# Performance work log

Hardware: AMD Instinct MI355X
Metric: run time of the kernel (lower is better)

## Reference

```python
import jax, jax.numpy as jnp
import numpy as np

D = 16      # core_size
R = 8       # rank
SIZE = D ** 3  # 4096, nr_cores = 3


def setup_inputs() -> dict:
    key = jax.random.key(0)
    k = jax.random.split(key, 5)
    core_std = np.sqrt(2.0 / D).astype(np.float32)  # kaiming_normal over (-1, d, d)
    x = jax.random.normal(k[0], (8, 1024, SIZE), dtype=jnp.float32)
    core0 = core_std * jax.random.normal(k[1], (D, D, D, D, R, 1), dtype=jnp.float32)
    core1 = core_std * jax.random.normal(k[2], (D, D, D, D, R, R), dtype=jnp.float32)
    core2 = core_std * jax.random.normal(k[3], (D, D, D, D, 1, R), dtype=jnp.float32)
    bias = np.sqrt(1.0 / SIZE).astype(np.float32) * jax.random.uniform(
        k[4], (SIZE,), dtype=jnp.float32, minval=-1.0, maxval=1.0)
    return {"x": x, "core0": core0, "core1": core1, "core2": core2, "bias": bias}


def to_matrix(core0, core1, core2):
    # Faithful translation of BTT.to_matrix for nr_cores=3.
    # G starts as core0: (d,d,d,d,r,1)
    # step idx=0 (core1): j=d, i=d^2
    c1 = core1.reshape(D, D * D, D, R, R)          # jixcb
    g = core0.reshape(D, D * D, D, R, 1)           # jiyba
    G = jnp.einsum('jixcb,jiyba->jiyxca', c1, g)   # (d, d^2, d, d, r, 1)
    # step idx=1 (core2): j=d^2, i=d
    c2 = core2.reshape(D * D, D, D, 1, R)          # jixcb
    g = G.reshape(D * D, D, D * D, R, 1)           # jiyba
    G = jnp.einsum('jixcb,jiyba->jiyxca', c2, g)   # (d^2, d, d^2, d, 1, 1)
    return G.reshape(SIZE, SIZE)


def reference(x, core0, core1, core2, bias):
    G = to_matrix(core0, core1, core2)
    out = x.reshape(-1, SIZE) @ G + bias
    return out.reshape(x.shape)
```

## Files before the change

kernel.cpp:

```cpp
#include <hip/hip_runtime.h>
#include <stdint.h>

typedef unsigned short u16;
typedef short bf16x8 __attribute__((ext_vector_type(8)));
typedef float f32x4 __attribute__((ext_vector_type(4)));
typedef u16 u16x4 __attribute__((ext_vector_type(4)));

__device__ __forceinline__ u16 f2bf(float f) {
    union { float f; unsigned int i; } v; v.f = f;
    unsigned int x = v.i;
    return (u16)((x + 0x7FFFu + ((x >> 16) & 1u)) >> 16);
}

__device__ __forceinline__ void async_load16(const u16* g, u16* lds) {
    __builtin_amdgcn_global_load_lds(
        (const __attribute__((address_space(1))) unsigned int*)g,
        (__attribute__((address_space(3))) unsigned int*)lds,
        16, 0, 0);
}

__global__ void transpose_cores(const float* __restrict__ c0, const float* __restrict__ c1,
                                const float* __restrict__ c2, float* __restrict__ c0t,
                                float* __restrict__ c1t, float* __restrict__ c2t) {
    __shared__ float t[64][65];
    int b = blockIdx.x;
    const float* in; float* outp; int Q, qt, rt;
    if (b < 1024)      { in = c1; outp = c1t; Q = 1024; qt = b & 15;          rt = b >> 4; }
    else if (b < 1152) { b -= 1024; in = c0; outp = c0t; Q = 128; qt = b & 1; rt = b >> 1; }
    else               { b -= 1152; in = c2; outp = c2t; Q = 128; qt = b & 1; rt = b >> 1; }
    const int r0 = rt * 64, q0 = qt * 64;
    const int tx = threadIdx.x & 63, ty = threadIdx.x >> 6;
    #pragma unroll
    for (int k = 0; k < 16; ++k)
        t[k * 4 + ty][tx] = in[(size_t)(r0 + k * 4 + ty) * Q + q0 + tx];
    __syncthreads();
    #pragma unroll
    for (int k = 0; k < 16; ++k)
        outp[(size_t)(q0 + k * 4 + ty) * 4096 + r0 + tx] = t[tx][k * 4 + ty];
}

__global__ __launch_bounds__(256, 1)
void build_gt_reuse(const float* __restrict__ c0t, const float* __restrict__ c1t,
                    const float* __restrict__ c2t, u16* __restrict__ Gt) {
    const int x1 = blockIdx.x;
    const int r  = blockIdx.y * 256 + threadIdx.x;

    float c1v[64];
    #pragma unroll
    for (int q = 0; q < 64; ++q)
        c1v[q] = c1t[(size_t)(x1 * 64 + q) * 4096 + r];

    #pragma unroll
    for (int yh = 0; yh < 2; ++yh) {
        float t[8][8];
        #pragma unroll
        for (int yy = 0; yy < 8; ++yy) {
            const int y1 = yh * 8 + yy;
            float a0[8];
            #pragma unroll
            for (int b = 0; b < 8; ++b)
                a0[b] = c0t[(size_t)(y1 * 8 + b) * 4096 + r];
            #pragma unroll
            for (int c = 0; c < 8; ++c) {
                float s = 0.f;
                #pragma unroll
                for (int b = 0; b < 8; ++b) s += c1v[c * 8 + b] * a0[b];
                t[yy][c] = s;
            }
        }
        #pragma unroll
        for (int x2 = 0; x2 < 16; ++x2) {
            float c2v[8];
            #pragma unroll
            for (int c = 0; c < 8; ++c)
                c2v[c] = c2t[(size_t)(x2 * 8 + c) * 4096 + r];
            #pragma unroll
            for (int yy = 0; yy < 8; ++yy) {
                const int y1 = yh * 8 + yy;
                float s = 0.f;
                #pragma unroll
                for (int c = 0; c < 8; ++c) s += c2v[c] * t[yy][c];
                Gt[(size_t)((y1 * 16 + x1) * 16 + x2) * 4096 + r] = f2bf(s);
            }
        }
    }
}

__global__ void conv_x(const f32x4* __restrict__ x, u16* __restrict__ xb, int n4) {
    for (int i = blockIdx.x * 256 + threadIdx.x; i < n4; i += gridDim.x * 256) {
        f32x4 v = x[i];
        u16x4 o;
        #pragma unroll
        for (int j = 0; j < 4; ++j) o[j] = f2bf(v[j]);
        *(u16x4*)(xb + 4 * (size_t)i) = o;
    }
}

__global__ __launch_bounds__(512, 2)
void gemm_8ph(const u16* __restrict__ Xb, const u16* __restrict__ Gt,
              const float* __restrict__ bias, float* __restrict__ out) {
    constexpr int K = 4096, N = 4096, NT = 64;
    extern __shared__ u16 lds[];

    const int tid  = threadIdx.x;
    const int lane = tid & 63;
    const int w    = tid >> 6;
    const int wmi  = w >> 2;
    const int wni  = w & 3;
    const int lr   = lane & 15;
    const int lq   = lane >> 4;
    const int xr   = lr & 7;

    int id = blockIdx.y * 16 + blockIdx.x;
    id = (id & 7) * 64 + (id >> 3);
    const int m0 = (id & 31) * 256;
    const int n0 = (id >> 5) * 256;

    const int r0 = tid >> 3;
    const int s0 = (tid & 7) ^ (r0 & 7);
    const int r1 = 64 + r0;
    const int s1 = ((512 + tid) & 7) ^ (r1 & 7);
    const size_t aoff0 = (size_t)(m0 + r0) * K + s0 * 8;
    const size_t aoff1 = (size_t)(m0 + r1) * K + s1 * 8;
    const size_t boff0 = (size_t)(n0 + r0) * K + s0 * 8;
    const size_t boff1 = (size_t)(n0 + r1) * K + s1 * 8;
    const int ldsw0 = (tid & ~63) * 8;
    const int ldsw1 = 4096 + (tid & ~63) * 8;

    const int aoffL = (wmi * 16 + lr) * 64;
    const int boffL = 16384 + (wni * 16 + lr) * 64;
    const int slot0 = (lq ^ xr) * 8;
    const int slot1 = ((4 + lq) ^ xr) * 8;

    f32x4 acc[8][4] = {};
    bf16x8 a[4][2];
    bf16x8 bfr[2][2][2];

    auto stageA = [&](int bb, int h, int t) {
        const u16* s = Xb + (size_t)h * (128 * K) + (size_t)t * 64;
        u16* d = lds + bb * 32768 + h * 8192;
        async_load16(s + aoff0, d + ldsw0);
        async_load16(s + aoff1, d + ldsw1);
    };
    auto stageB = [&](int bb, int h, int t) {
        const u16* s = Gt + (size_t)h * (128 * K) + (size_t)t * 64;
        u16* d = lds + bb * 32768 + 16384 + h * 8192;
        async_load16(s + boff0, d + ldsw0);
        async_load16(s + boff1, d + ldsw1);
    };
    auto loadA = [&](int bb, int h) {
        const u16* p = lds + bb * 32768 + h * 8192 + aoffL;
        #pragma unroll
        for (int li = 0; li < 4; ++li) {
            a[li][0] = *(const bf16x8*)(p + li * 2048 + slot0);
            a[li][1] = *(const bf16x8*)(p + li * 2048 + slot1);
        }
    };
    auto loadB = [&](int bb, int h) {
        const u16* p = lds + bb * 32768 + h * 8192 + boffL;
        #pragma unroll
        for (int lj = 0; lj < 2; ++lj) {
            bfr[h][lj][0] = *(const bf16x8*)(p + lj * 4096 + slot0);
            bfr[h][lj][1] = *(const bf16x8*)(p + lj * 4096 + slot1);
        }
    };
    auto mfmaQ = [&](int mh, int nh) {
        #pragma unroll
        for (int li = 0; li < 4; ++li)
            #pragma unroll
            for (int lj = 0; lj < 2; ++lj) {
                f32x4 c = acc[mh * 4 + li][nh * 2 + lj];
                c = __builtin_amdgcn_mfma_f32_16x16x32_bf16(a[li][0], bfr[nh][lj][0], c, 0, 0, 0);
                c = __builtin_amdgcn_mfma_f32_16x16x32_bf16(a[li][1], bfr[nh][lj][1], c, 0, 0, 0);
                acc[mh * 4 + li][nh * 2 + lj] = c;
            }
    };
    auto mfmaQ_refillA = [&](int mh, int nh, const u16* pA) {
        #pragma unroll
        for (int li = 0; li < 4; ++li) {
            #pragma unroll
            for (int lj = 0; lj < 2; ++lj) {
                f32x4 c = acc[mh * 4 + li][nh * 2 + lj];
                c = __builtin_amdgcn_mfma_f32_16x16x32_bf16(a[li][0], bfr[nh][lj][0], c, 0, 0, 0);
                c = __builtin_amdgcn_mfma_f32_16x16x32_bf16(a[li][1], bfr[nh][lj][1], c, 0, 0, 0);
                acc[mh * 4 + li][nh * 2 + lj] = c;
            }
            a[li][0] = *(const bf16x8*)(pA + li * 2048 + slot0);
            a[li][1] = *(const bf16x8*)(pA + li * 2048 + slot1);
        }
    };

    stageA(0, 0, 0); stageB(0, 0, 0); stageA(0, 1, 0); stageB(0, 1, 0);
    stageA(1, 0, 1); stageB(1, 0, 1); stageA(1, 1, 1); stageB(1, 1, 1);
    asm volatile("s_waitcnt vmcnt(8)" ::: "memory");
    __builtin_amdgcn_s_barrier();
    loadB(0, 1); loadA(0, 0); loadB(0, 0);

    for (int T = 0; T < NT; ++T) {
        const int bc = T & 1, bn = bc ^ 1;
        const int t2 = (T + 2) & (NT - 1);

        asm volatile("s_waitcnt lgkmcnt(0)" ::: "memory");
        __builtin_amdgcn_s_barrier();
        __builtin_amdgcn_sched_barrier(0);
        __builtin_amdgcn_s_setprio(1);
        mfmaQ(0, 0);
        __builtin_amdgcn_s_setprio(0);

        stageA(bc, 0, t2); stageB(bc, 0, t2);
        __builtin_amdgcn_s_setprio(1);
        mfmaQ_refillA(0, 1, lds + bc * 32768 + 8192 + aoffL);
        __builtin_amdgcn_s_setprio(0);

        asm volatile("s_waitcnt lgkmcnt(0)" ::: "memory");
        __builtin_amdgcn_s_barrier();
        __builtin_amdgcn_sched_barrier(0);
        __builtin_amdgcn_s_setprio(1);
        mfmaQ(1, 1);
        __builtin_amdgcn_s_setprio(0);

        stageA(bc, 1, t2); stageB(bc, 1, t2);
        asm volatile("s_waitcnt vmcnt(8)" ::: "memory");
        __builtin_amdgcn_s_barrier();
        __builtin_amdgcn_sched_barrier(0);
        loadB(bn, 1);
        __builtin_amdgcn_s_setprio(1);
        mfmaQ_refillA(1, 0, lds + bn * 32768 + aoffL);
        __builtin_amdgcn_s_setprio(0);
        loadB(bn, 0);
    }
    asm volatile("s_waitcnt vmcnt(0) lgkmcnt(0)" ::: "memory");

    #pragma unroll
    for (int j = 0; j < 4; ++j) {
        const int n = n0 + (j * 4 + wni) * 16 + lr;
        const float bv = bias[n];
        #pragma unroll
        for (int i = 0; i < 8; ++i) {
            const int mb = m0 + (2 * i + wmi) * 16 + lq * 4;
            #pragma unroll
            for (int r = 0; r < 4; ++r)
                out[(size_t)(mb + r) * N + n] = acc[i][j][r] + bv;
        }
    }
}

__global__ void build_gt(const float* __restrict__ c0, const float* __restrict__ c1,
                         const float* __restrict__ c2, u16* __restrict__ Gt) {
    const int y1  = blockIdx.x >> 4;
    const int x1  = blockIdx.x & 15;
    const int r   = blockIdx.y * 256 + threadIdx.x;

    float a0[8];
    {
        f32x4 v0 = *(const f32x4*)(c0 + ((size_t)r * 16 + y1) * 8);
        f32x4 v1 = *(const f32x4*)(c0 + ((size_t)r * 16 + y1) * 8 + 4);
        #pragma unroll
        for (int b = 0; b < 4; ++b) { a0[b] = v0[b]; a0[4 + b] = v1[b]; }
    }
    float t[8];
    const float* c1row = c1 + ((size_t)r * 16 + x1) * 64;
    #pragma unroll
    for (int c = 0; c < 8; ++c) {
        f32x4 v0 = *(const f32x4*)(c1row + c * 8);
        f32x4 v1 = *(const f32x4*)(c1row + c * 8 + 4);
        float s = 0.f;
        #pragma unroll
        for (int b = 0; b < 4; ++b) s += v0[b] * a0[b] + v1[b] * a0[4 + b];
        t[c] = s;
    }
    const float* c2row = c2 + (size_t)r * 128;
    #pragma unroll
    for (int x2 = 0; x2 < 16; ++x2) {
        f32x4 v0 = *(const f32x4*)(c2row + x2 * 8);
        f32x4 v1 = *(const f32x4*)(c2row + x2 * 8 + 4);
        float s = 0.f;
        #pragma unroll
        for (int c = 0; c < 4; ++c) s += v0[c] * t[c] + v1[c] * t[4 + c];
        Gt[((size_t)(blockIdx.x * 16 + x2)) * 4096 + r] = f2bf(s);
    }
}

#define TM 128
#define TN 128
#define BK 32

__global__ void gemm_bt_f32(const float* __restrict__ Xf, const u16* __restrict__ Gt,
                            const float* __restrict__ bias, float* __restrict__ out) {
    constexpr int K = 4096, N = 4096;
    __shared__ __attribute__((aligned(16))) u16 As[TM * BK];
    __shared__ __attribute__((aligned(16))) u16 Bs[TN * BK];

    const int tid  = threadIdx.x;
    const int lane = tid & 63;
    const int w    = tid >> 6;
    const int m0   = blockIdx.y * TM;
    const int n0   = blockIdx.x * TN;
    const int wm   = (w >> 1) * 64;
    const int wn   = (w & 1) * 64;
    const int lr   = lane & 15;
    const int lk   = (lane >> 4) * 8;

    f32x4 acc[4][4] = {};

    const int srow   = tid >> 2;
    const int schunk = (tid & 3) * 8;
    const u16* grow0 = Gt + (size_t)(n0 + srow) * K + schunk;
    const u16* grow1 = Gt + (size_t)(n0 + 64 + srow) * K + schunk;
    u16* ldsB0 = &Bs[(tid & ~63) * 8];
    u16* ldsB1 = &Bs[(256 + (tid & ~63)) * 8];

    const float* xsrc = Xf + (size_t)(m0 + (tid >> 1)) * K + (tid & 1) * 16;
    u16* adst = &As[(tid >> 1) * BK + (tid & 1) * 16];

    for (int k0 = 0; k0 < K; k0 += BK) {
        __syncthreads();
        {
            f32x4 v0 = ((const f32x4*)(xsrc + k0))[0];
            f32x4 v1 = ((const f32x4*)(xsrc + k0))[1];
            f32x4 v2 = ((const f32x4*)(xsrc + k0))[2];
            f32x4 v3 = ((const f32x4*)(xsrc + k0))[3];
            bf16x8 w0, w1;
            #pragma unroll
            for (int j = 0; j < 4; ++j) {
                w0[j]     = (short)f2bf(v0[j]);
                w0[4 + j] = (short)f2bf(v1[j]);
                w1[j]     = (short)f2bf(v2[j]);
                w1[4 + j] = (short)f2bf(v3[j]);
            }
            *(bf16x8*)adst = w0;
            *(bf16x8*)(adst + 8) = w1;
        }
        async_load16(grow0 + k0, ldsB0);
        async_load16(grow1 + k0, ldsB1);
        __syncthreads();

        bf16x8 af[4], bg[4];
        #pragma unroll
        for (int i = 0; i < 4; ++i) {
            af[i] = *(const bf16x8*)(&As[(wm + i * 16 + lr) * BK + lk]);
            bg[i] = *(const bf16x8*)(&Bs[(wn + i * 16 + lr) * BK + lk]);
        }
        #pragma unroll
        for (int mt = 0; mt < 4; ++mt)
            #pragma unroll
            for (int nt = 0; nt < 4; ++nt)
                acc[mt][nt] = __builtin_amdgcn_mfma_f32_16x16x32_bf16(
                    af[mt], bg[nt], acc[mt][nt], 0, 0, 0);
    }

    #pragma unroll
    for (int nt = 0; nt < 4; ++nt) {
        const int n = n0 + wn + nt * 16 + lr;
        const float bv = bias[n];
        #pragma unroll
        for (int mt = 0; mt < 4; ++mt) {
            const int mbase = m0 + wm + mt * 16 + (lane >> 4) * 4;
            #pragma unroll
            for (int r = 0; r < 4; ++r) {
                out[(size_t)(mbase + r) * N + n] = acc[mt][nt][r] + bv;
            }
        }
    }
}

extern "C" void kernel_launch(void* const* d_in, const int* in_sizes, int n_in,
                              void* d_out, int out_size, void* d_ws, size_t ws_size,
                              hipStream_t stream) {
    const float* x    = (const float*)d_in[0];
    const float* c0   = (const float*)d_in[1];
    const float* c1   = (const float*)d_in[2];
    const float* c2   = (const float*)d_in[3];
    const float* bias = (const float*)d_in[4];
    float* out = (float*)d_out;

    const size_t GT_BYTES   = (size_t)4096 * 4096 * sizeof(u16);
    const size_t XB_BYTES   = (size_t)8192 * 4096 * sizeof(u16);
    const size_t CORE_BYTES = (size_t)20 * 1024 * 1024;
    u16* Gt = (u16*)d_ws;

    if (ws_size >= GT_BYTES + XB_BYTES) {
        u16* Xb = (u16*)((char*)d_ws + GT_BYTES);
        static int attr_done = 0;
        if (!attr_done) {
            hipFuncSetAttribute(reinterpret_cast<const void*>(gemm_8ph),
                                hipFuncAttributeMaxDynamicSharedMemorySize, 131072);
            attr_done = 1;
        }

        float* c1t; float* c0t; float* c2t;
        if (ws_size >= GT_BYTES + XB_BYTES + CORE_BYTES) {
            char* cores = (char*)d_ws + GT_BYTES + XB_BYTES;
            c1t = (float*)cores;
            c0t = (float*)(cores + (size_t)16 * 1024 * 1024);
            c2t = (float*)(cores + (size_t)18 * 1024 * 1024);
        } else {
            char* scratch = (char*)d_ws + GT_BYTES;
            c1t = (float*)scratch;
            c0t = (float*)(scratch + (size_t)16 * 1024 * 1024);
            c2t = (float*)(scratch + (size_t)18 * 1024 * 1024);
        }
        transpose_cores<<<1280, 256, 0, stream>>>(c0, c1, c2, c0t, c1t, c2t);
        build_gt_reuse<<<dim3(16, 16), 256, 0, stream>>>(c0t, c1t, c2t, Gt);
        conv_x<<<8192, 256, 0, stream>>>((const f32x4*)x, Xb, 8192 * 4096 / 4);
        gemm_8ph<<<dim3(16, 32), 512, 131072, stream>>>(Xb, Gt, bias, out);
    } else {
        build_gt<<<dim3(256, 16), 256, 0, stream>>>(c0, c1, c2, Gt);
        gemm_bt_f32<<<dim3(32, 64), 256, 0, stream>>>(x, Gt, bias, out);
    }
}
```

Measured before the change: 498.1 us.

## Restructure LDS fragment loads to overlap with MFMA and move barriers after compute

Splits the A-fragment LDS reads into two halves. The second half and the B high fragment are now issued at the start of each quadrant instead of being waited on before a barrier. The waitcnt/barrier pairs move after the MFMA quadrants so LDS reads overlap with matrix math rather than stalling before it. This adds register pressure and depends on the compiler keeping MFMA and LDS reads interleaved without the sched_barrier fences. It could also introduce hazards if a buffer is overwritten before the moved barriers are reached.

```diff
diff --git a/kernel.cpp b/kernel.cpp
--- a/kernel.cpp
+++ b/kernel.cpp
@@ -148,13 +148,17 @@
         async_load16(s + boff0, d + ldsw0);
         async_load16(s + boff1, d + ldsw1);
     };
-    auto loadA = [&](int bb, int h) {
-        const u16* p = lds + bb * 32768 + h * 8192 + aoffL;
-        #pragma unroll
-        for (int li = 0; li < 4; ++li) {
-            a[li][0] = *(const bf16x8*)(p + li * 2048 + slot0);
-            a[li][1] = *(const bf16x8*)(p + li * 2048 + slot1);
-        }
+    auto loadA01 = [&](const u16* pA) {
+        a[0][0] = *(const bf16x8*)(pA + slot0);
+        a[0][1] = *(const bf16x8*)(pA + slot1);
+        a[1][0] = *(const bf16x8*)(pA + 2048 + slot0);
+        a[1][1] = *(const bf16x8*)(pA + 2048 + slot1);
+    };
+    auto loadA23 = [&](const u16* pA) {
+        a[2][0] = *(const bf16x8*)(pA + 2 * 2048 + slot0);
+        a[2][1] = *(const bf16x8*)(pA + 2 * 2048 + slot1);
+        a[3][0] = *(const bf16x8*)(pA + 3 * 2048 + slot0);
+        a[3][1] = *(const bf16x8*)(pA + 3 * 2048 + slot1);
     };
     auto loadB = [&](int bb, int h) {
         const u16* p = lds + bb * 32768 + h * 8192 + boffL;
@@ -175,7 +179,7 @@
                 acc[mh * 4 + li][nh * 2 + lj] = c;
             }
     };
-    auto mfmaQ_refillA = [&](int mh, int nh, const u16* pA) {
+    auto mfmaQ_r01 = [&](int mh, int nh, const u16* pA) {
         #pragma unroll
         for (int li = 0; li < 4; ++li) {
             #pragma unroll
@@ -185,8 +189,10 @@
                 c = __builtin_amdgcn_mfma_f32_16x16x32_bf16(a[li][1], bfr[nh][lj][1], c, 0, 0, 0);
                 acc[mh * 4 + li][nh * 2 + lj] = c;
             }
-            a[li][0] = *(const bf16x8*)(pA + li * 2048 + slot0);
-            a[li][1] = *(const bf16x8*)(pA + li * 2048 + slot1);
+            if (li < 2) {
+                a[li][0] = *(const bf16x8*)(pA + li * 2048 + slot0);
+                a[li][1] = *(const bf16x8*)(pA + li * 2048 + slot1);
+            }
         }
     };
 
@@ -194,38 +200,40 @@
     stageA(1, 0, 1); stageB(1, 0, 1); stageA(1, 1, 1); stageB(1, 1, 1);
     asm volatile("s_waitcnt vmcnt(8)" ::: "memory");
     __builtin_amdgcn_s_barrier();
-    loadB(0, 1); loadA(0, 0); loadB(0, 0);
+    loadA01(lds + aoffL);
+    loadB(0, 0);
 
     for (int T = 0; T < NT; ++T) {
         const int bc = T & 1, bn = bc ^ 1;
         const int t2 = (T + 2) & (NT - 1);
-
-        asm volatile("s_waitcnt lgkmcnt(0)" ::: "memory");
-        __builtin_amdgcn_s_barrier();
-        __builtin_amdgcn_sched_barrier(0);
+        const u16* pc = lds + bc * 32768;
+
+        loadB(bc, 1);
+        loadA23(pc + aoffL);
         __builtin_amdgcn_s_setprio(1);
         mfmaQ(0, 0);
         __builtin_amdgcn_s_setprio(0);
+        asm volatile("s_waitcnt lgkmcnt(0)" ::: "memory");
+        __builtin_amdgcn_s_barrier();
 
         stageA(bc, 0, t2); stageB(bc, 0, t2);
         __builtin_amdgcn_s_setprio(1);
-        mfmaQ_refillA(0, 1, lds + bc * 32768 + 8192 + aoffL);
+        mfmaQ_r01(0, 1, pc + 8192 + aoffL);
         __builtin_amdgcn_s_setprio(0);
 
-        asm volatile("s_waitcnt lgkmcnt(0)" ::: "memory");
-        __builtin_amdgcn_s_barrier();
-        __builtin_amdgcn_sched_barrier(0);
+        loadA23(pc + 8192 + aoffL);
         __builtin_amdgcn_s_setprio(1);
         mfmaQ(1, 1);
         __builtin_amdgcn_s_setprio(0);
+        asm volatile("s_waitcnt lgkmcnt(0)" ::: "memory");
+        __builtin_amdgcn_s_barrier();
 
         stageA(bc, 1, t2); stageB(bc, 1, t2);
         asm volatile("s_waitcnt vmcnt(8)" ::: "memory");
         __builtin_amdgcn_s_barrier();
         __builtin_amdgcn_sched_barrier(0);
-        loadB(bn, 1);
         __builtin_amdgcn_s_setprio(1);
-        mfmaQ_refillA(1, 0, lds + bn * 32768 + aoffL);
+        mfmaQ_r01(1, 0, lds + bn * 32768 + aoffL);
         __builtin_amdgcn_s_setprio(0);
         loadB(bn, 0);
     }
```

Result: no change. 500.0 us (+0.4%).
